# Kernel tuning notes

Measured on AMD Instinct MI355X. Metric: run time of the kernel, lower is better.

## Reference

```python
import jax, jax.numpy as jnp
import numpy as np

N_NODES = 100000
N_EDGES = 3200000
IN_DIM = 512
HID_DIM = 16


def spmm(edge_src, edge_dst, edge_weight, feats):
    # out[i] = sum_{(j->i) in E} w_e * feats[j]  (sparse adj @ feats)
    gathered = feats[edge_src] * edge_weight[:, None]  # [E, D]
    return jax.ops.segment_sum(gathered, edge_dst, num_segments=N_NODES)


def setup_inputs() -> dict:
    key = jax.random.key(0)
    ks = jax.random.split(key, 8)
    x = jax.random.normal(ks[0], (N_NODES, IN_DIM), dtype=jnp.float32)
    edge_src = jax.random.randint(ks[1], (N_EDGES,), 0, N_NODES, dtype=jnp.int32)
    edge_dst = jax.random.randint(ks[2], (N_EDGES,), 0, N_NODES, dtype=jnp.int32)
    # normalized adjacency weights (positive, small, like D^-1/2 A D^-1/2 entries)
    edge_weight = jax.random.uniform(ks[3], (N_EDGES,), dtype=jnp.float32) * 0.1
    # Glorot-style init for GraphConvolution weights
    W1 = jax.random.normal(ks[4], (IN_DIM, HID_DIM), dtype=jnp.float32) * (1.0 / np.sqrt(IN_DIM))
    b1 = jnp.zeros((HID_DIM,), dtype=jnp.float32)
    W2 = jax.random.normal(ks[5], (HID_DIM, 1), dtype=jnp.float32) * (1.0 / np.sqrt(HID_DIM))
    b2 = jnp.zeros((1,), dtype=jnp.float32)
    return {"x": x, "edge_src": edge_src, "edge_dst": edge_dst,
            "edge_weight": edge_weight, "W1": W1, "b1": b1, "W2": W2, "b2": b2}


def reference(x, edge_src, edge_dst, edge_weight, W1, b1, W2, b2):
    # Layer 1: GraphConvolution(input_dim -> hidden_dim) + ReLU
    h = spmm(edge_src, edge_dst, edge_weight, x @ W1) + b1  # [N, 16]
    h = jax.nn.relu(h)
    # dropout is identity in eval mode (training=False)
    # Layer 2: GraphConvolution(hidden_dim -> 1)
    out = spmm(edge_src, edge_dst, edge_weight, h @ W2) + b2  # [N, 1]
    return out
```

## Files before the change

kernel.cpp:

```cpp
#include <hip/hip_runtime.h>
#include <hip/hip_fp16.h>

#define N_NODES 100000
#define N_EDGES 3200000
#define IN_DIM  512
#define HID_DIM 16

#define B_BKT   782
#define BKT_SH  7
#define EPB2    5000
#define NBLK2   640
#define CAP_MAX 4608

#define G1_TILES 6250
#define G1_BLK   782
#define MERGED_SMEM 61440

typedef __attribute__((ext_vector_type(8))) short bf16x8;
typedef __attribute__((ext_vector_type(4))) float f32x4;

__device__ __forceinline__ void atomic_add_f32(float* p, float v) {
    __hip_atomic_fetch_add(p, v, __ATOMIC_RELAXED, __HIP_MEMORY_SCOPE_AGENT);
}
__device__ __forceinline__ int atomic_add_i32(int* p, int v) {
    return __hip_atomic_fetch_add(p, v, __ATOMIC_RELAXED, __HIP_MEMORY_SCOPE_AGENT);
}

__device__ __forceinline__ unsigned short bf16_rne(float f) {
    unsigned u = __float_as_uint(f);
    return (unsigned short)((u + 0x7fffu + ((u >> 16) & 1u)) >> 16);
}

__global__ void z0_init(int* __restrict__ cursor, int cap) {
    int b = blockIdx.x * blockDim.x + threadIdx.x;
    if (b < B_BKT) cursor[b] = b * cap;
}

__global__ __launch_bounds__(512) void m1_gs(const float* __restrict__ x,
                                             const float* __restrict__ W1,
                                             __half* __restrict__ xwh,
                                             const int* __restrict__ src,
                                             const int* __restrict__ dst,
                                             const float* __restrict__ wgt,
                                             int* __restrict__ cursor,
                                             uint2* __restrict__ rec, int cap) {
    extern __shared__ __align__(16) char smem[];
    const int t = threadIdx.x;

    if (blockIdx.x < NBLK2) {
        uint2*          srt   = (uint2*)smem;
        unsigned short* bkt   = (unsigned short*)(smem + 40000);
        int*            hist  = (int*)(smem + 50000);
        int*            lbase = (int*)(smem + 53128);
        int*            gbase = (int*)(smem + 56256);
        int*            scn   = (int*)(smem + 59384);

        for (int b = t; b < B_BKT; b += 512) hist[b] = 0;
        __syncthreads();

        const int e0 = blockIdx.x * EPB2;
        const int4*   d4 = (const int4*)(dst + e0);
        const int4*   s4 = (const int4*)(src + e0);
        const float4* w4 = (const float4*)(wgt + e0);
        const int NG = EPB2 / 4;

        for (int g = t; g < NG; g += 512) {
            int4 d = d4[g];
            atomicAdd(&hist[d.x >> BKT_SH], 1);
            atomicAdd(&hist[d.y >> BKT_SH], 1);
            atomicAdd(&hist[d.z >> BKT_SH], 1);
            atomicAdd(&hist[d.w >> BKT_SH], 1);
        }
        __syncthreads();

        int c0 = 0, c1 = 0;
        if (t < 391) { c0 = hist[2 * t]; c1 = hist[2 * t + 1]; }
        int s = c0 + c1;
        scn[t] = s;
        __syncthreads();
        for (int off = 1; off < 512; off <<= 1) {
            int v = (t >= off) ? scn[t - off] : 0;
            __syncthreads();
            scn[t] += v;
            __syncthreads();
        }
        int excl = scn[t] - s;
        if (t < 391) {
            lbase[2 * t]     = excl;
            lbase[2 * t + 1] = excl + c0;
        }
        __syncthreads();

        for (int b = t; b < B_BKT; b += 512) {
            int c = hist[b];
            gbase[b] = c > 0 ? atomic_add_i32(&cursor[b], c) : 0;
        }
        __syncthreads();
        for (int b = t; b < B_BKT; b += 512) hist[b] = lbase[b];
        __syncthreads();

        for (int g = t; g < NG; g += 512) {
            int4 d = d4[g];
            int4 sv = s4[g];
            float4 w = w4[g];
            {
                int b = d.x >> BKT_SH;
                int pos = atomicAdd(&hist[b], 1);
                srt[pos] = make_uint2(((unsigned)sv.x << BKT_SH) | (unsigned)(d.x & 127),
                                      __float_as_uint(w.x));
                bkt[pos] = (unsigned short)b;
            }
            {
                int b = d.y >> BKT_SH;
                int pos = atomicAdd(&hist[b], 1);
                srt[pos] = make_uint2(((unsigned)sv.y << BKT_SH) | (unsigned)(d.y & 127),
                                      __float_as_uint(w.y));
                bkt[pos] = (unsigned short)b;
            }
            {
                int b = d.z >> BKT_SH;
                int pos = atomicAdd(&hist[b], 1);
                srt[pos] = make_uint2(((unsigned)sv.z << BKT_SH) | (unsigned)(d.z & 127),
                                      __float_as_uint(w.z));
                bkt[pos] = (unsigned short)b;
            }
            {
                int b = d.w >> BKT_SH;
                int pos = atomicAdd(&hist[b], 1);
                srt[pos] = make_uint2(((unsigned)sv.w << BKT_SH) | (unsigned)(d.w & 127),
                                      __float_as_uint(w.w));
                bkt[pos] = (unsigned short)b;
            }
        }
        __syncthreads();

        for (int i = t; i < EPB2; i += 512) {
            int b = bkt[i];
            rec[gbase[b] + (i - lbase[b])] = srt[i];
        }
    } else {
        unsigned short* whi = (unsigned short*)smem;
        unsigned short* wlo = (unsigned short*)(smem + 16384);

        for (int idx = t; idx < 16 * 64 * 8; idx += 512) {
            int c  = idx >> 9;
            int l  = (idx >> 3) & 63;
            int tt = idx & 7;
            int k  = c * 32 + ((l >> 4) << 3) + tt;
            int j  = l & 15;
            float w = W1[k * HID_DIM + j];
            unsigned u = __float_as_uint(w);
            float hif = __uint_as_float(u & 0xffff0000u);
            whi[idx] = (unsigned short)(u >> 16);
            wlo[idx] = bf16_rne(w - hif);
        }
        __syncthreads();

        const int lane = t & 63;
        const int wid  = (blockIdx.x - NBLK2) * 8 + (t >> 6);
        if (wid >= G1_TILES) return;
        const int row0 = wid * 16;

        const float* xrow = x + (size_t)(row0 + (lane & 15)) * IN_DIM + ((lane >> 4) << 3);
        const unsigned short* whp = &whi[lane * 8];
        const unsigned short* wlp = &wlo[lane * 8];

        f32x4 acc = {0.f, 0.f, 0.f, 0.f};
        float4 p0[2], p1[2];
        p0[0] = *(const float4*)(xrow);
        p1[0] = *(const float4*)(xrow + 4);
        p0[1] = *(const float4*)(xrow + 32);
        p1[1] = *(const float4*)(xrow + 36);
#pragma unroll
        for (int c = 0; c < 16; ++c) {
            const int cur = c & 1;
            float4 n0, n1;
            if (c < 14) {
                n0 = *(const float4*)(xrow + (c + 2) * 32);
                n1 = *(const float4*)(xrow + (c + 2) * 32 + 4);
            }
            float av[8] = {p0[cur].x, p0[cur].y, p0[cur].z, p0[cur].w,
                           p1[cur].x, p1[cur].y, p1[cur].z, p1[cur].w};
            bf16x8 ah, al;
#pragma unroll
            for (int e = 0; e < 8; ++e) {
                unsigned u = __float_as_uint(av[e]);
                ah[e] = (short)(u >> 16);
                float lof = av[e] - __uint_as_float(u & 0xffff0000u);
                al[e] = (short)bf16_rne(lof);
            }
            bf16x8 bh = *(const bf16x8*)(whp + (size_t)c * 512);
            bf16x8 bl = *(const bf16x8*)(wlp + (size_t)c * 512);
            acc = __builtin_amdgcn_mfma_f32_16x16x32_bf16(ah, bh, acc, 0, 0, 0);
            acc = __builtin_amdgcn_mfma_f32_16x16x32_bf16(al, bh, acc, 0, 0, 0);
            acc = __builtin_amdgcn_mfma_f32_16x16x32_bf16(ah, bl, acc, 0, 0, 0);
            if (c < 14) { p0[cur] = n0; p1[cur] = n1; }
        }

        const int n     = lane & 15;
        const int rbase = row0 + ((lane >> 4) << 2);
#pragma unroll
        for (int i = 0; i < 4; ++i)
            xwh[(size_t)(rbase + i) * HID_DIM + n] = __float2half_rn(acc[i]);
    }
}

__global__ __launch_bounds__(256) void g1_xw_mfma(const float* __restrict__ x,
                                                  const float* __restrict__ W1,
                                                  __half* __restrict__ xwh) {
    __shared__ alignas(16) unsigned short whi[16 * 64 * 8];
    __shared__ alignas(16) unsigned short wlo[16 * 64 * 8];
    const int t = threadIdx.x;

    for (int idx = t; idx < 16 * 64 * 8; idx += 256) {
        int c  = idx >> 9;
        int l  = (idx >> 3) & 63;
        int tt = idx & 7;
        int k  = c * 32 + ((l >> 4) << 3) + tt;
        int j  = l & 15;
        float w = W1[k * HID_DIM + j];
        unsigned u = __float_as_uint(w);
        float hif = __uint_as_float(u & 0xffff0000u);
        whi[idx] = (unsigned short)(u >> 16);
        wlo[idx] = bf16_rne(w - hif);
    }
    __syncthreads();

    const int lane = t & 63;
    const int wid  = blockIdx.x * 4 + (t >> 6);
    if (wid >= G1_TILES) return;
    const int row0 = wid * 16;

    const float* xrow = x + (size_t)(row0 + (lane & 15)) * IN_DIM + ((lane >> 4) << 3);
    const unsigned short* whp = &whi[lane * 8];
    const unsigned short* wlp = &wlo[lane * 8];

    f32x4 acc = {0.f, 0.f, 0.f, 0.f};
    float4 p0[2], p1[2];
    p0[0] = *(const float4*)(xrow);
    p1[0] = *(const float4*)(xrow + 4);
    p0[1] = *(const float4*)(xrow + 32);
    p1[1] = *(const float4*)(xrow + 36);
#pragma unroll
    for (int c = 0; c < 16; ++c) {
        const int cur = c & 1;
        float4 n0, n1;
        if (c < 14) {
            n0 = *(const float4*)(xrow + (c + 2) * 32);
            n1 = *(const float4*)(xrow + (c + 2) * 32 + 4);
        }
        float av[8] = {p0[cur].x, p0[cur].y, p0[cur].z, p0[cur].w,
                       p1[cur].x, p1[cur].y, p1[cur].z, p1[cur].w};
        bf16x8 ah, al;
#pragma unroll
        for (int e = 0; e < 8; ++e) {
            unsigned u = __float_as_uint(av[e]);
            ah[e] = (short)(u >> 16);
            float lof = av[e] - __uint_as_float(u & 0xffff0000u);
            al[e] = (short)bf16_rne(lof);
        }
        bf16x8 bh = *(const bf16x8*)(whp + (size_t)c * 512);
        bf16x8 bl = *(const bf16x8*)(wlp + (size_t)c * 512);
        acc = __builtin_amdgcn_mfma_f32_16x16x32_bf16(ah, bh, acc, 0, 0, 0);
        acc = __builtin_amdgcn_mfma_f32_16x16x32_bf16(al, bh, acc, 0, 0, 0);
        acc = __builtin_amdgcn_mfma_f32_16x16x32_bf16(ah, bl, acc, 0, 0, 0);
        if (c < 14) { p0[cur] = n0; p1[cur] = n1; }
    }

    const int n     = lane & 15;
    const int rbase = row0 + ((lane >> 4) << 2);
#pragma unroll
    for (int i = 0; i < 4; ++i)
        xwh[(size_t)(rbase + i) * HID_DIM + n] = __float2half_rn(acc[i]);
}

__global__ __launch_bounds__(512) void s2p4(const int* __restrict__ cursor,
                                            uint2* __restrict__ rec,
                                            int2* __restrict__ row,
                                            const __half* __restrict__ xwh,
                                            const float* __restrict__ b1,
                                            const float* __restrict__ W2,
                                            float* __restrict__ hw, int cap) {
    __shared__ uint2 srt[CAP_MAX];
    __shared__ int ocnt[128], scn[128], cur[128];
    const int t = threadIdx.x;
    const int bkt = blockIdx.x;
    const int e0 = bkt * cap;
    int n = cursor[bkt] - e0;
    n = max(0, min(n, cap));
    if (t < 128) ocnt[t] = 0;
    __syncthreads();
    for (int i = t; i < n; i += 512)
        atomicAdd(&ocnt[rec[e0 + i].x & 127u], 1);
    __syncthreads();
    if (t < 128) scn[t] = ocnt[t];
    __syncthreads();
    for (int off = 1; off < 128; off <<= 1) {
        int v = 0;
        if (t < 128 && t >= off) v = scn[t - off];
        __syncthreads();
        if (t < 128 && t >= off) scn[t] += v;
        __syncthreads();
    }
    if (t < 128) {
        int b = scn[t] - ocnt[t];
        cur[t] = b;
        int node = (bkt << BKT_SH) + t;
        if (node < N_NODES) row[node] = make_int2(e0 + b, ocnt[t]);
    }
    __syncthreads();
    for (int i = t; i < n; i += 512) {
        uint2 r = rec[e0 + i];
        int d = (int)(r.x & 127u);
        int pos = atomicAdd(&cur[d], 1);
        srt[pos] = make_uint2(r.x >> BKT_SH, r.y);
    }
    __syncthreads();
    for (int i = t; i < n; i += 512) rec[e0 + i] = srt[i];
    const int j = t & 15;
    for (int g = (t >> 4); g < 128; g += 32) {
        const int node = (bkt << BKT_SH) + g;
        if (node >= N_NODES) continue;
        int e = scn[g] - ocnt[g];
        const int end = scn[g];
        float acc = 0.0f;
        for (; e + 4 <= end; e += 4) {
            uint2 q0 = srt[e], q1 = srt[e + 1], q2 = srt[e + 2], q3 = srt[e + 3];
            float f0 = __half2float(xwh[(size_t)q0.x * HID_DIM + j]);
            float f1 = __half2float(xwh[(size_t)q1.x * HID_DIM + j]);
            float f2 = __half2float(xwh[(size_t)q2.x * HID_DIM + j]);
            float f3 = __half2float(xwh[(size_t)q3.x * HID_DIM + j]);
            acc += __uint_as_float(q0.y) * f0;
            acc += __uint_as_float(q1.y) * f1;
            acc += __uint_as_float(q2.y) * f2;
            acc += __uint_as_float(q3.y) * f3;
        }
        for (; e < end; ++e) {
            uint2 q = srt[e];
            acc += __uint_as_float(q.y) * __half2float(xwh[(size_t)q.x * HID_DIM + j]);
        }
        float v = fmaxf(acc + b1[j], 0.0f) * W2[j];
        v += __shfl_xor(v, 1);
        v += __shfl_xor(v, 2);
        v += __shfl_xor(v, 4);
        v += __shfl_xor(v, 8);
        if (j == 0) hw[node] = v;
    }
}

__global__ __launch_bounds__(256) void p5_layer2(const int2* __restrict__ row,
                                                 const uint2* __restrict__ rec,
                                                 const float* __restrict__ hwv,
                                                 const float* __restrict__ b2,
                                                 float* __restrict__ out) {
    const int t = threadIdx.x;
    const int node = blockIdx.x * 32 + (t >> 3);
    const int i = t & 7;
    int2 r = row[node];
    const int end = r.x + r.y;
    int k = r.x + i;
    float s = 0.0f;
    for (; k + 24 < end; k += 32) {
        uint2 a = rec[k], b = rec[k + 8], c = rec[k + 16], d = rec[k + 24];
        float ha = hwv[a.x], hb = hwv[b.x], hc = hwv[c.x], hd = hwv[d.x];
        s += __uint_as_float(a.y) * ha + __uint_as_float(b.y) * hb
           + __uint_as_float(c.y) * hc + __uint_as_float(d.y) * hd;
    }
    for (; k < end; k += 8) {
        uint2 a = rec[k];
        s += __uint_as_float(a.y) * hwv[a.x];
    }
    s += __shfl_xor(s, 1);
    s += __shfl_xor(s, 2);
    s += __shfl_xor(s, 4);
    if (i == 0) out[node] = b2[0] + s;
}

__global__ void f0_zero(float* __restrict__ h, const float* __restrict__ b2,
                        float* __restrict__ out) {
    int i = blockIdx.x * blockDim.x + threadIdx.x;
    if (i < N_NODES * HID_DIM) h[i] = 0.0f;
    if (i < N_NODES) out[i] = b2[0];
}
__global__ void k2_spmm1(const int* __restrict__ src, const int* __restrict__ dst,
                         const float* __restrict__ wgt, const __half* __restrict__ xwh,
                         float* __restrict__ h) {
    int t = blockIdx.x * blockDim.x + threadIdx.x;
    int e = t >> 4;
    int j = t & (HID_DIM - 1);
    if (e < N_EDGES) {
        float v = wgt[e] * __half2float(xwh[(size_t)src[e] * HID_DIM + j]);
        atomic_add_f32(&h[(size_t)dst[e] * HID_DIM + j], v);
    }
}
__global__ void k3_act(const float* __restrict__ h, const float* __restrict__ b1,
                       const float* __restrict__ W2, float* __restrict__ hw) {
    int i = blockIdx.x * blockDim.x + threadIdx.x;
    if (i >= N_NODES) return;
    const float4* h4 = (const float4*)(h + (size_t)i * HID_DIM);
    const float4* b4 = (const float4*)b1;
    const float4* w4 = (const float4*)W2;
    float acc = 0.0f;
#pragma unroll
    for (int q = 0; q < HID_DIM / 4; ++q) {
        float4 hv = h4[q]; float4 bv = b4[q]; float4 wv = w4[q];
        acc += fmaxf(hv.x + bv.x, 0.0f) * wv.x;
        acc += fmaxf(hv.y + bv.y, 0.0f) * wv.y;
        acc += fmaxf(hv.z + bv.z, 0.0f) * wv.z;
        acc += fmaxf(hv.w + bv.w, 0.0f) * wv.w;
    }
    hw[i] = acc;
}
__global__ void k4_spmm2(const int* __restrict__ src, const int* __restrict__ dst,
                         const float* __restrict__ wgt, const float* __restrict__ hw,
                         float* __restrict__ out) {
    int e = blockIdx.x * blockDim.x + threadIdx.x;
    if (e < N_EDGES) atomic_add_f32(&out[dst[e]], wgt[e] * hw[src[e]]);
}


extern "C" void kernel_launch(void* const* d_in, const int* in_sizes, int n_in,
                              void* d_out, int out_size, void* d_ws, size_t ws_size,
                              hipStream_t stream) {
    const float* x    = (const float*)d_in[0];
    const int*   esrc = (const int*)  d_in[1];
    const int*   edst = (const int*)  d_in[2];
    const float* ew   = (const float*)d_in[3];
    const float* W1   = (const float*)d_in[4];
    const float* b1   = (const float*)d_in[5];
    const float* W2   = (const float*)d_in[6];
    const float* b2   = (const float*)d_in[7];
    float* out = (float*)d_out;
    char* ws = (char*)d_ws;

    __half* xwh    = (__half*)ws;
    float*  hw     = (float*)(ws + (size_t)N_NODES * HID_DIM * 2);
    int*    cursor = (int*)(hw + N_NODES);
    int2*   row    = (int2*)(((size_t)(cursor + B_BKT) + 7) & ~(size_t)7);
    size_t rec_off = ((size_t)((char*)(row + N_NODES) - ws) + 15) & ~(size_t)15;
    uint2* rec = (uint2*)(ws + rec_off);

    int cap = 0;
    if (ws_size > rec_off) {
        size_t cap_fit = (ws_size - rec_off) / ((size_t)B_BKT * sizeof(uint2));
        cap = (int)(cap_fit < CAP_MAX ? cap_fit : CAP_MAX);
    }

    if (cap >= 4480) {
        z0_init<<<(B_BKT + 255) / 256, 256, 0, stream>>>(cursor, cap);
        m1_gs<<<NBLK2 + G1_BLK, 512, MERGED_SMEM, stream>>>(x, W1, xwh,
                                                            esrc, edst, ew,
                                                            cursor, rec, cap);
        s2p4<<<B_BKT, 512, 0, stream>>>(cursor, rec, row, xwh, b1, W2, hw, cap);
        p5_layer2<<<N_NODES / 32, 256, 0, stream>>>(row, rec, hw, b2, out);
    } else {
        __half* f_xwh = (__half*)ws;
        float*  f_h   = (float*)(ws + (size_t)N_NODES * HID_DIM * 2);
        float*  f_hw  = f_h + (size_t)N_NODES * HID_DIM;
        int n = N_NODES * HID_DIM;
        f0_zero<<<(n + 255) / 256, 256, 0, stream>>>(f_h, b2, out);
        g1_xw_mfma<<<(G1_TILES + 3) / 4, 256, 0, stream>>>(x, W1, f_xwh);
        k2_spmm1<<<(N_EDGES * 16) / 256, 256, 0, stream>>>(esrc, edst, ew, f_xwh, f_h);
        k3_act<<<(N_NODES + 255) / 256, 256, 0, stream>>>(f_h, b1, W2, f_hw);
        k4_spmm2<<<(N_EDGES + 255) / 256, 256, 0, stream>>>(esrc, edst, ew, f_hw, out);
    }
}
```

Baseline: 392.9 us.

## Keep bucket records in registers, drop sorted writeback, bucket-local layer-2 reduction

```diff
diff --git a/kernel.cpp b/kernel.cpp
--- a/kernel.cpp
+++ b/kernel.cpp
@@ -11,6 +11,7 @@
 #define EPB2    5000
 #define NBLK2   640
 #define CAP_MAX 4608
+#define RSTG    9
 
 #define G1_TILES 6250
 #define G1_BLK   782
@@ -274,13 +275,12 @@
         xwh[(size_t)(rbase + i) * HID_DIM + n] = __float2half_rn(acc[i]);
 }
 
-__global__ __launch_bounds__(512) void s2p4(const int* __restrict__ cursor,
-                                            uint2* __restrict__ rec,
-                                            int2* __restrict__ row,
-                                            const __half* __restrict__ xwh,
-                                            const float* __restrict__ b1,
-                                            const float* __restrict__ W2,
-                                            float* __restrict__ hw, int cap) {
+__global__ __launch_bounds__(512) void s2p4b(const int* __restrict__ cursor,
+                                             const uint2* __restrict__ rec,
+                                             const __half* __restrict__ xwh,
+                                             const float* __restrict__ b1,
+                                             const float* __restrict__ W2,
+                                             float* __restrict__ hw, int cap) {
     __shared__ uint2 srt[CAP_MAX];
     __shared__ int ocnt[128], scn[128], cur[128];
     const int t = threadIdx.x;
@@ -290,9 +290,18 @@
     n = max(0, min(n, cap));
     if (t < 128) ocnt[t] = 0;
     __syncthreads();
-    for (int i = t; i < n; i += 512)
-        atomicAdd(&ocnt[rec[e0 + i].x & 127u], 1);
-    __syncthreads();
+
+    uint2 rg[RSTG];
+#pragma unroll
+    for (int q = 0; q < RSTG; ++q) {
+        int i = t + q * 512;
+        if (i < n) {
+            rg[q] = rec[e0 + i];
+            atomicAdd(&ocnt[rg[q].x & 127u], 1);
+        }
+    }
+    __syncthreads();
+
     if (t < 128) scn[t] = ocnt[t];
     __syncthreads();
     for (int off = 1; off < 128; off <<= 1) {
@@ -302,21 +311,21 @@
         if (t < 128 && t >= off) scn[t] += v;
         __syncthreads();
     }
-    if (t < 128) {
-        int b = scn[t] - ocnt[t];
-        cur[t] = b;
-        int node = (bkt << BKT_SH) + t;
-        if (node < N_NODES) row[node] = make_int2(e0 + b, ocnt[t]);
-    }
-    __syncthreads();
-    for (int i = t; i < n; i += 512) {
-        uint2 r = rec[e0 + i];
-        int d = (int)(r.x & 127u);
-        int pos = atomicAdd(&cur[d], 1);
-        srt[pos] = make_uint2(r.x >> BKT_SH, r.y);
-    }
-    __syncthreads();
-    for (int i = t; i < n; i += 512) rec[e0 + i] = srt[i];
+    if (t < 128) cur[t] = scn[t] - ocnt[t];
+    __syncthreads();
+
+#pragma unroll
+    for (int q = 0; q < RSTG; ++q) {
+        int i = t + q * 512;
+        if (i < n) {
+            uint2 r = rg[q];
+            int d = (int)(r.x & 127u);
+            int pos = atomicAdd(&cur[d], 1);
+            srt[pos] = make_uint2(r.x >> BKT_SH, r.y);
+        }
+    }
+    __syncthreads();
+
     const int j = t & 15;
     for (int g = (t >> 4); g < 128; g += 32) {
         const int node = (bkt << BKT_SH) + g;
@@ -324,6 +333,26 @@
         int e = scn[g] - ocnt[g];
         const int end = scn[g];
         float acc = 0.0f;
+        for (; e + 8 <= end; e += 8) {
+            uint2 q0 = srt[e],     q1 = srt[e + 1], q2 = srt[e + 2], q3 = srt[e + 3];
+            uint2 q4 = srt[e + 4], q5 = srt[e + 5], q6 = srt[e + 6], q7 = srt[e + 7];
+            float f0 = __half2float(xwh[(size_t)q0.x * HID_DIM + j]);
+            float f1 = __half2float(xwh[(size_t)q1.x * HID_DIM + j]);
+            float f2 = __half2float(xwh[(size_t)q2.x * HID_DIM + j]);
+            float f3 = __half2float(xwh[(size_t)q3.x * HID_DIM + j]);
+            float f4 = __half2float(xwh[(size_t)q4.x * HID_DIM + j]);
+            float f5 = __half2float(xwh[(size_t)q5.x * HID_DIM + j]);
+            float f6 = __half2float(xwh[(size_t)q6.x * HID_DIM + j]);
+            float f7 = __half2float(xwh[(size_t)q7.x * HID_DIM + j]);
+            acc += __uint_as_float(q0.y) * f0;
+            acc += __uint_as_float(q1.y) * f1;
+            acc += __uint_as_float(q2.y) * f2;
+            acc += __uint_as_float(q3.y) * f3;
+            acc += __uint_as_float(q4.y) * f4;
+            acc += __uint_as_float(q5.y) * f5;
+            acc += __uint_as_float(q6.y) * f6;
+            acc += __uint_as_float(q7.y) * f7;
+        }
         for (; e + 4 <= end; e += 4) {
             uint2 q0 = srt[e], q1 = srt[e + 1], q2 = srt[e + 2], q3 = srt[e + 3];
             float f0 = __half2float(xwh[(size_t)q0.x * HID_DIM + j]);
@@ -348,32 +377,37 @@
     }
 }
 
-__global__ __launch_bounds__(256) void p5_layer2(const int2* __restrict__ row,
-                                                 const uint2* __restrict__ rec,
-                                                 const float* __restrict__ hwv,
-                                                 const float* __restrict__ b2,
-                                                 float* __restrict__ out) {
+__global__ __launch_bounds__(512) void p5c(const int* __restrict__ cursor,
+                                           const uint2* __restrict__ rec,
+                                           const float* __restrict__ hwv,
+                                           const float* __restrict__ b2,
+                                           float* __restrict__ out, int cap) {
+    __shared__ float o[128];
     const int t = threadIdx.x;
-    const int node = blockIdx.x * 32 + (t >> 3);
-    const int i = t & 7;
-    int2 r = row[node];
-    const int end = r.x + r.y;
-    int k = r.x + i;
-    float s = 0.0f;
-    for (; k + 24 < end; k += 32) {
-        uint2 a = rec[k], b = rec[k + 8], c = rec[k + 16], d = rec[k + 24];
-        float ha = hwv[a.x], hb = hwv[b.x], hc = hwv[c.x], hd = hwv[d.x];
-        s += __uint_as_float(a.y) * ha + __uint_as_float(b.y) * hb
-           + __uint_as_float(c.y) * hc + __uint_as_float(d.y) * hd;
-    }
-    for (; k < end; k += 8) {
-        uint2 a = rec[k];
-        s += __uint_as_float(a.y) * hwv[a.x];
-    }
-    s += __shfl_xor(s, 1);
-    s += __shfl_xor(s, 2);
-    s += __shfl_xor(s, 4);
-    if (i == 0) out[node] = b2[0] + s;
+    const int bkt = blockIdx.x;
+    const int e0 = bkt * cap;
+    int n = cursor[bkt] - e0;
+    n = max(0, min(n, cap));
+    if (t < 128) o[t] = 0.0f;
+    __syncthreads();
+    const uint4* r4 = (const uint4*)(rec + e0);
+    const int m = n >> 1;
+    for (int i = t; i < m; i += 512) {
+        uint4 q = r4[i];
+        float v0 = __uint_as_float(q.y) * hwv[q.x >> BKT_SH];
+        float v1 = __uint_as_float(q.w) * hwv[q.z >> BKT_SH];
+        atomicAdd(&o[q.x & 127u], v0);
+        atomicAdd(&o[q.z & 127u], v1);
+    }
+    if ((n & 1) && t == 0) {
+        uint2 q = rec[e0 + n - 1];
+        atomicAdd(&o[q.x & 127u], __uint_as_float(q.y) * hwv[q.x >> BKT_SH]);
+    }
+    __syncthreads();
+    if (t < 128) {
+        int node = (bkt << BKT_SH) + t;
+        if (node < N_NODES) out[node] = b2[0] + o[t];
+    }
 }
 
 __global__ void f0_zero(float* __restrict__ h, const float* __restrict__ b2,
@@ -439,6 +473,7 @@
     int2*   row    = (int2*)(((size_t)(cursor + B_BKT) + 7) & ~(size_t)7);
     size_t rec_off = ((size_t)((char*)(row + N_NODES) - ws) + 15) & ~(size_t)15;
     uint2* rec = (uint2*)(ws + rec_off);
+    (void)row;
 
     int cap = 0;
     if (ws_size > rec_off) {
@@ -451,8 +486,8 @@
         m1_gs<<<NBLK2 + G1_BLK, 512, MERGED_SMEM, stream>>>(x, W1, xwh,
                                                             esrc, edst, ew,
                                                             cursor, rec, cap);
-        s2p4<<<B_BKT, 512, 0, stream>>>(cursor, rec, row, xwh, b1, W2, hw, cap);
-        p5_layer2<<<N_NODES / 32, 256, 0, stream>>>(row, rec, hw, b2, out);
+        s2p4b<<<B_BKT, 512, 0, stream>>>(cursor, rec, xwh, b1, W2, hw, cap);
+        p5c<<<B_BKT, 512, 0, stream>>>(cursor, rec, hw, b2, out, cap);
     } else {
         __half* f_xwh = (__half*)ws;
         float*  f_h   = (float*)(ws + (size_t)N_NODES * HID_DIM * 2);
```

After: 395.7 us. About the same (+0.7%).
